# Kernel tuning notes

Hardware: AMD Instinct MI355X
Metric: run time of the kernel (lower is better)

The kernel has to match this reference:

```python
import jax, jax.numpy as jnp
import numpy as np
from functools import partial

N_NODES = 100000
IN_FEATS = 64
HIDDEN = 32
N_EDGES = 3200000


def gcn_conv(x, edge_index, W, b, num_nodes):
    """PyG GCNConv: x' = D^-1/2 (A+I) D^-1/2 (x W) + b, degrees include self-loops."""
    xw = x @ W  # [N, H]
    loop = jnp.arange(num_nodes, dtype=edge_index.dtype)
    src = jnp.concatenate([edge_index[0], loop])
    dst = jnp.concatenate([edge_index[1], loop])
    deg = jax.ops.segment_sum(jnp.ones_like(dst, dtype=xw.dtype), dst,
                              num_segments=num_nodes)  # in-degree incl. self-loop
    dinv = jnp.where(deg > 0, jax.lax.rsqrt(deg), 0.0)
    norm = dinv[src] * dinv[dst]  # [E+N]
    msg = xw[src] * norm[:, None]  # gather + scale
    out = jax.ops.segment_sum(msg, dst, num_segments=num_nodes)  # scatter-add
    return out + b


def setup_inputs() -> dict:
    key = jax.random.key(0)
    ks = jax.random.split(key, 6)
    scale = 1.0 / np.sqrt(IN_FEATS)
    return {
        "x_house": jax.random.normal(ks[0], (N_NODES, IN_FEATS), dtype=jnp.float32),
        "edge_index_near": jax.random.randint(ks[1], (2, N_EDGES), 0, N_NODES, dtype=jnp.int64)
            if jax.config.jax_enable_x64 else jax.random.randint(ks[1], (2, N_EDGES), 0, N_NODES).astype(jnp.int32),
        "edge_index_similar": jax.random.randint(ks[2], (2, N_EDGES), 0, N_NODES).astype(jnp.int32),
        "W_near": jax.random.normal(ks[3], (IN_FEATS, HIDDEN), dtype=jnp.float32) * scale,
        "b_near": jnp.zeros((HIDDEN,), dtype=jnp.float32),
        "W_similar": jax.random.normal(ks[4], (IN_FEATS, HIDDEN), dtype=jnp.float32) * scale,
        "b_similar": jnp.zeros((HIDDEN,), dtype=jnp.float32),
        "W_lin": jax.random.normal(ks[5], (HIDDEN, 1), dtype=jnp.float32) * (1.0 / np.sqrt(HIDDEN)),
        "b_lin": jnp.zeros((1,), dtype=jnp.float32),
    }


def reference(x_house, edge_index_near, edge_index_similar,
              W_near, b_near, W_similar, b_similar, W_lin, b_lin):
    # HeteroConv with aggr='sum': sum of per-edge-type GCNConv outputs on 'house'
    h = (gcn_conv(x_house, edge_index_near, W_near, b_near, N_NODES)
         + gcn_conv(x_house, edge_index_similar, W_similar, b_similar, N_NODES))
    h = jax.nn.relu(h)
    # dropout is identity at inference (training=False)
    out = h @ W_lin + b_lin  # [N, 1]
    return out.squeeze(-1)
```

## Files before the change

### kernel.cpp

```cpp
#include <hip/hip_runtime.h>
#include <hip/hip_fp16.h>


#define SLICES 256
#define BSZ    256
#define NB_MAX 800
#define CAP2   9216
#define PCH    4096
#define LDSPAD 33
#define FXS    65536.0f
#define FXSI   (1.0f / 65536.0f)

__global__ __launch_bounds__(512)
void init_kernel(const float* __restrict__ Wn, const float* __restrict__ Ws,
                 int* __restrict__ goff, float* __restrict__ wtn,
                 float* __restrict__ wts, int nb) {
    const int t = threadIdx.x;
    for (int b = t; b < nb; b += 512) goff[b] = 0;
    for (int i = t; i < 64 * 32; i += 512) {
        int k = i >> 5, h = i & 31;
        wtn[h * 64 + k] = Wn[i];
        wts[h * 64 + k] = Ws[i];
    }
}

__global__ __launch_bounds__(512)
void place_kernel(const int* __restrict__ ei_n, const int* __restrict__ ei_s,
                  int* __restrict__ goff, unsigned int* __restrict__ codes,
                  int En, int Es, int nb) {
    __shared__ unsigned stg[PCH];
    __shared__ unsigned stg2[PCH];
    __shared__ int histT[NB_MAX];
    __shared__ int cur[NB_MAX];
    __shared__ int histC[NB_MAX];
    __shared__ int baseC[NB_MAX];
    __shared__ int gbC[NB_MAX];
    __shared__ int wsum[8];
    const int t = threadIdx.x;
    const int wid = t >> 6, lane = t & 63;
    const int type = blockIdx.y;
    const int* __restrict__ ei = type ? ei_s : ei_n;
    const int E = type ? Es : En;
    int per = ((E + SLICES - 1) / SLICES + 7) & ~7;
    const int e0 = blockIdx.x * per;
    const int e1 = min(e0 + per, E);

    for (int b = t; b < nb; b += 512) histT[b] = 0;
    __syncthreads();

    for (int c0 = e0; c0 < e1; c0 += PCH) {
        const int i = c0 + t * 8;
        int nv = e1 - i; nv = nv < 0 ? 0 : (nv > 8 ? 8 : nv);
        if (nv == 8) {
            int4 dA = *(const int4*)(ei + E + i), dB = *(const int4*)(ei + E + i + 4);
            atomicAdd(&histT[dA.x >> 7], 1);
            atomicAdd(&histT[dA.y >> 7], 1);
            atomicAdd(&histT[dA.z >> 7], 1);
            atomicAdd(&histT[dA.w >> 7], 1);
            atomicAdd(&histT[dB.x >> 7], 1);
            atomicAdd(&histT[dB.y >> 7], 1);
            atomicAdd(&histT[dB.z >> 7], 1);
            atomicAdd(&histT[dB.w >> 7], 1);
        } else {
            for (int j = 0; j < nv; ++j) atomicAdd(&histT[ei[E + i + j] >> 7], 1);
        }
    }
    __syncthreads();

    for (int b = t; b < nb; b += 512) {
        int c = histT[b];
        cur[b] = b * CAP2 + (c ? atomicAdd(&goff[b], c) : 0);
    }
    for (int b = t; b < nb; b += 512) histC[b] = 0;
    __syncthreads();

    for (int c0 = e0; c0 < e1; c0 += PCH) {
        const int i = c0 + t * 8;
        int nv = e1 - i; nv = nv < 0 ? 0 : (nv > 8 ? 8 : nv);
        unsigned cd[8]; int bb[8], rk[8];
        if (nv == 8) {
            int4 sA = *(const int4*)(ei + i),     sB = *(const int4*)(ei + i + 4);
            int4 dA = *(const int4*)(ei + E + i), dB = *(const int4*)(ei + E + i + 4);
            int ss[8] = {sA.x, sA.y, sA.z, sA.w, sB.x, sB.y, sB.z, sB.w};
            int dd[8] = {dA.x, dA.y, dA.z, dA.w, dB.x, dB.y, dB.z, dB.w};
#pragma unroll
            for (int j = 0; j < 8; ++j) {
                bb[j] = dd[j] >> 7;
                cd[j] = ((unsigned)(2 * (dd[j] & 127) + type) << 18)
                      | (unsigned)(2 * ss[j] + type);
            }
        } else {
            for (int j = 0; j < nv; ++j) {
                int sv = ei[i + j], dv = ei[E + i + j];
                bb[j] = dv >> 7;
                cd[j] = ((unsigned)(2 * (dv & 127) + type) << 18)
                      | (unsigned)(2 * sv + type);
            }
        }
#pragma unroll
        for (int j = 0; j < 8; ++j)
            if (j < nv) rk[j] = atomicAdd(&histC[bb[j]], 1);
        __syncthreads();

        const int i0 = wid * 128 + lane, i1 = i0 + 64;
        int v0 = (i0 < nb) ? histC[i0] : 0;
        int v1 = (i1 < nb) ? histC[i1] : 0;
        int x0 = v0;
#pragma unroll
        for (int o = 1; o < 64; o <<= 1) { int n = __shfl_up(x0, o, 64); if (lane >= o) x0 += n; }
        int tot0 = __shfl(x0, 63, 64);
        int x1 = v1;
#pragma unroll
        for (int o = 1; o < 64; o <<= 1) { int n = __shfl_up(x1, o, 64); if (lane >= o) x1 += n; }
        int tot1 = __shfl(x1, 63, 64);
        if (lane == 0) wsum[wid] = tot0 + tot1;
        for (int b = t; b < nb; b += 512) {
            int c = histC[b], g = cur[b];
            gbC[b] = g;
            cur[b] = g + c;
        }
        __syncthreads();
        int woff = 0;
#pragma unroll
        for (int k = 0; k < 8; ++k) woff += (k < wid) ? wsum[k] : 0;
        if (i0 < nb) baseC[i0] = woff + (x0 - v0);
        if (i1 < nb) baseC[i1] = woff + tot0 + (x1 - v1);
        __syncthreads();

#pragma unroll
        for (int j = 0; j < 8; ++j)
            if (j < nv) {
                int p = baseC[bb[j]] + rk[j];
                stg[p] = cd[j];
                stg2[p] = (unsigned)(gbC[bb[j]] + rk[j]);
            }
        __syncthreads();

        const int tot = min(PCH, e1 - c0);
        for (int j = t; j < tot; j += 512)
            codes[stg2[j]] = stg[j];
        for (int b = t; b < nb; b += 512) histC[b] = 0;
        __syncthreads();
    }
}

__global__ __launch_bounds__(256)
void dcxw_kernel(const unsigned int* __restrict__ codes, const int* __restrict__ goff,
                 const float* __restrict__ x,
                 const float* __restrict__ wtn, const float* __restrict__ wts,
                 int* __restrict__ cnt, __half2* __restrict__ xws, int N, int M, int nb) {
    __shared__ int dcnt[512];
    const int t = threadIdx.x;
    dcnt[t] = 0;
    dcnt[t + 256] = 0;
    __syncthreads();

    for (int bb = 0; bb < 2; ++bb) {
        const int bidx = 2 * blockIdx.x + bb;
        if (bidx >= nb) break;
        const int off = bb << 8;
        const int base = bidx * CAP2;
        const int end = base + goff[bidx];
        const int t0 = base + ((end - base) & ~3);
        for (int e = base + t * 4; e < t0; e += 256 * 4) {
            uint4 c = *(const uint4*)(codes + e);
            atomicAdd(&dcnt[off + (c.x >> 18)], 1);
            atomicAdd(&dcnt[off + (c.y >> 18)], 1);
            atomicAdd(&dcnt[off + (c.z >> 18)], 1);
            atomicAdd(&dcnt[off + (c.w >> 18)], 1);
        }
        if (t < end - t0) atomicAdd(&dcnt[off + (codes[t0 + t] >> 18)], 1);
    }
    __syncthreads();

    const int v0 = blockIdx.x * 512 + t;
    if (v0 < M) cnt[v0] = dcnt[t];
    const int v1 = v0 + 256;
    if (v1 < M) cnt[v1] = dcnt[t + 256];

    const int node = blockIdx.x * 256 + t;
    if (node >= N) return;

    float xr[64];
    const float4* x4 = (const float4*)(x + (size_t)node * 64);
#pragma unroll
    for (int q = 0; q < 16; ++q) {
        float4 v = x4[q];
        xr[4 * q] = v.x; xr[4 * q + 1] = v.y; xr[4 * q + 2] = v.z; xr[4 * q + 3] = v.w;
    }
    float dn = rsqrtf((float)dcnt[2 * t] + 1.0f);
    float ds = rsqrtf((float)dcnt[2 * t + 1] + 1.0f);

    const float4* wn4 = (const float4*)wtn;
    const float4* ws4 = (const float4*)wts;

    unsigned pn[16], ps[16];
#pragma unroll
    for (int s2 = 0; s2 < 16; ++s2) {
        float a0n = 0.f, a1n = 0.f, a0s = 0.f, a1s = 0.f;
#pragma unroll
        for (int q = 0; q < 16; ++q) {
            float4 w0n = wn4[(2 * s2) * 16 + q];
            float4 w1n = wn4[(2 * s2 + 1) * 16 + q];
            float4 w0s = ws4[(2 * s2) * 16 + q];
            float4 w1s = ws4[(2 * s2 + 1) * 16 + q];
            float x0 = xr[4 * q], x1 = xr[4 * q + 1], x2 = xr[4 * q + 2], x3 = xr[4 * q + 3];
            a0n += x0 * w0n.x + x1 * w0n.y + x2 * w0n.z + x3 * w0n.w;
            a1n += x0 * w1n.x + x1 * w1n.y + x2 * w1n.z + x3 * w1n.w;
            a0s += x0 * w0s.x + x1 * w0s.y + x2 * w0s.z + x3 * w0s.w;
            a1s += x0 * w1s.x + x1 * w1s.y + x2 * w1s.z + x3 * w1s.w;
        }
        __half2 hn = __floats2half2_rn(a0n * dn, a1n * dn);
        __half2 hs = __floats2half2_rn(a0s * ds, a1s * ds);
        pn[s2] = *(unsigned*)&hn;
        ps[s2] = *(unsigned*)&hs;
    }
    uint4* on = (uint4*)(xws + (size_t)(2 * node) * 16);
    uint4* os = (uint4*)(xws + (size_t)(2 * node + 1) * 16);
#pragma unroll
    for (int q = 0; q < 4; ++q) {
        on[q] = make_uint4(pn[4 * q], pn[4 * q + 1], pn[4 * q + 2], pn[4 * q + 3]);
        os[q] = make_uint4(ps[4 * q], ps[4 * q + 1], ps[4 * q + 2], ps[4 * q + 3]);
    }
}

__global__ __launch_bounds__(1024)
void gather_kernel(const unsigned int* __restrict__ codes, const int* __restrict__ goff,
                   const __half2* __restrict__ xws, const int* __restrict__ cnt,
                   const float* __restrict__ b_n, const float* __restrict__ b_s,
                   const float* __restrict__ W_lin, const float* __restrict__ b_lin,
                   float* __restrict__ out, int N) {
    __shared__ int facc[BSZ * LDSPAD];
    for (int i = threadIdx.x; i < BSZ * LDSPAD; i += 1024) facc[i] = 0;
    __syncthreads();
    const int b = blockIdx.x;
    const int base = b * CAP2;
    const int end = base + goff[b];
    const int sl = threadIdx.x & 15;
    const int grp = threadIdx.x >> 4;

#define GA(cc) xws[(size_t)((cc) & 0x3FFFFu) * 16 + sl]
#define ACC_EDGE(cc, ww) do {                                                \
        float2 f_ = __half22float2(ww);                                      \
        int r_ = (int)((cc) >> 18) * LDSPAD + sl;                            \
        atomicAdd(&facc[r_],      __float2int_rn(f_.x * FXS));               \
        atomicAdd(&facc[r_ + 16], __float2int_rn(f_.y * FXS));               \
    } while (0)

    const int t0 = base + ((end - base) & ~15);
    for (int e = base + grp * 16; e < t0; e += 64 * 16) {
        uint4 c0 = *(const uint4*)(codes + e);
        uint4 c1 = *(const uint4*)(codes + e + 4);
        uint4 c2 = *(const uint4*)(codes + e + 8);
        uint4 c3 = *(const uint4*)(codes + e + 12);
        __half2 w0 = GA(c0.x), w1 = GA(c0.y), w2 = GA(c0.z), w3 = GA(c0.w);
        __half2 w4 = GA(c1.x), w5 = GA(c1.y), w6 = GA(c1.z), w7 = GA(c1.w);
        __half2 w8 = GA(c2.x), w9 = GA(c2.y), wA = GA(c2.z), wB = GA(c2.w);
        __half2 wC = GA(c3.x), wD = GA(c3.y), wE = GA(c3.z), wF = GA(c3.w);
        ACC_EDGE(c0.x, w0); ACC_EDGE(c0.y, w1); ACC_EDGE(c0.z, w2); ACC_EDGE(c0.w, w3);
        ACC_EDGE(c1.x, w4); ACC_EDGE(c1.y, w5); ACC_EDGE(c1.z, w6); ACC_EDGE(c1.w, w7);
        ACC_EDGE(c2.x, w8); ACC_EDGE(c2.y, w9); ACC_EDGE(c2.z, wA); ACC_EDGE(c2.w, wB);
        ACC_EDGE(c3.x, wC); ACC_EDGE(c3.y, wD); ACC_EDGE(c3.z, wE); ACC_EDGE(c3.w, wF);
    }
    for (int e = t0 + grp; e < end; e += 64) {
        unsigned c = codes[e];
        __half2 w = GA(c);
        ACC_EDGE(c, w);
    }
#undef ACC_EDGE
#undef GA

    __syncthreads();
    const float bn0 = b_n[2 * sl], bn1 = b_n[2 * sl + 1];
    const float bs0 = b_s[2 * sl], bs1 = b_s[2 * sl + 1];
    const float wl0 = W_lin[2 * sl], wl1 = W_lin[2 * sl + 1];
    const float bl  = b_lin[0];
    for (int p = grp; p < 128; p += 64) {
        int node = b * 128 + p;
        if (node >= N) break;
        int rn = (2 * p) * LDSPAD, rs = rn + LDSPAD;
        float anx = (float)facc[rn + sl] * FXSI, any_ = (float)facc[rn + 16 + sl] * FXSI;
        float asx = (float)facc[rs + sl] * FXSI, asy  = (float)facc[rs + 16 + sl] * FXSI;
        float2 ns = __half22float2(xws[(size_t)(2 * node) * 16 + sl]);
        float2 ss = __half22float2(xws[(size_t)(2 * node + 1) * 16 + sl]);
        float dn  = rsqrtf((float)cnt[2 * node] + 1.0f);
        float dsv = rsqrtf((float)cnt[2 * node + 1] + 1.0f);
        float h0 = (anx + ns.x) * dn + bn0 + (asx + ss.x) * dsv + bs0;
        float h1 = (any_ + ns.y) * dn + bn1 + (asy + ss.y) * dsv + bs1;
        float pr = fmaxf(h0, 0.f) * wl0 + fmaxf(h1, 0.f) * wl1;
#pragma unroll
        for (int off = 8; off > 0; off >>= 1) pr += __shfl_xor(pr, off, 16);
        if (sl == 0) out[node] = pr + bl;
    }
}

extern "C" void kernel_launch(void* const* d_in, const int* in_sizes, int n_in,
                              void* d_out, int out_size, void* d_ws, size_t ws_size,
                              hipStream_t stream) {
    const float* x     = (const float*)d_in[0];
    const int*   ei_n  = (const int*)d_in[1];
    const int*   ei_s  = (const int*)d_in[2];
    const float* W_n   = (const float*)d_in[3];
    const float* b_n   = (const float*)d_in[4];
    const float* W_s   = (const float*)d_in[5];
    const float* b_s   = (const float*)d_in[6];
    const float* W_lin = (const float*)d_in[7];
    const float* b_lin = (const float*)d_in[8];
    float* out = (float*)d_out;

    const int N  = in_sizes[0] / 64;
    const int En = in_sizes[1] / 2;
    const int Es = in_sizes[2] / 2;
    const int M  = 2 * N;
    const int nb = (M + BSZ - 1) / BSZ;

    int*   goff = (int*)d_ws;
    int*   cnt  = goff + 1024;
    float* wtn  = (float*)(cnt + M);
    float* wts  = wtn + 2048;
    uintptr_t pc = (uintptr_t)(wts + 2048);
    pc = (pc + 15) & ~(uintptr_t)15;
    unsigned int* codes = (unsigned int*)pc;
    __half2* xws = (__half2*)(codes + (size_t)nb * CAP2);

    init_kernel<<<1, 512, 0, stream>>>(W_n, W_s, goff, wtn, wts, nb);
    place_kernel<<<dim3(SLICES, 2), 512, 0, stream>>>(ei_n, ei_s, goff, codes,
                                                      En, Es, nb);
    dcxw_kernel<<<(nb + 1) / 2, 256, 0, stream>>>(codes, goff, x, wtn, wts,
                                                  cnt, xws, N, M, nb);
    gather_kernel<<<nb, 1024, 0, stream>>>(codes, goff, xws, cnt,
                                           b_n, b_s, W_lin, b_lin, out, N);
}
```

Baseline: 287.6 us.

## Split degree count and XW into separate kernels with 16 lanes per node

Breaks the fused degree-count-plus-transform kernel into a degree-count kernel and an XW kernel. In the XW kernel each node is handled by 16 threads, each computing two output columns per edge type, with weights transposed into padded LDS. Previously one thread computed all 64 outputs from a 64-float register array with global weight loads. The init kernel is replaced by hipMemsetAsync, and the weight transpose moves into each block. This adds one kernel launch and a cnt round trip through global memory, and every thread of a node rereads the node's x row.

After: 282.7 us. No clear change (-1.7%).

```diff
diff --git a/kernel.cpp b/kernel.cpp
--- a/kernel.cpp
+++ b/kernel.cpp
@@ -8,21 +8,9 @@
 #define CAP2   9216
 #define PCH    4096
 #define LDSPAD 33
+#define WSTR   68
 #define FXS    65536.0f
 #define FXSI   (1.0f / 65536.0f)
-
-__global__ __launch_bounds__(512)
-void init_kernel(const float* __restrict__ Wn, const float* __restrict__ Ws,
-                 int* __restrict__ goff, float* __restrict__ wtn,
-                 float* __restrict__ wts, int nb) {
-    const int t = threadIdx.x;
-    for (int b = t; b < nb; b += 512) goff[b] = 0;
-    for (int i = t; i < 64 * 32; i += 512) {
-        int k = i >> 5, h = i & 31;
-        wtn[h * 64 + k] = Wn[i];
-        wts[h * 64 + k] = Ws[i];
-    }
-}
 
 __global__ __launch_bounds__(512)
 void place_kernel(const int* __restrict__ ei_n, const int* __restrict__ ei_s,
@@ -145,83 +133,68 @@
 }
 
 __global__ __launch_bounds__(256)
-void dcxw_kernel(const unsigned int* __restrict__ codes, const int* __restrict__ goff,
-                 const float* __restrict__ x,
-                 const float* __restrict__ wtn, const float* __restrict__ wts,
-                 int* __restrict__ cnt, __half2* __restrict__ xws, int N, int M, int nb) {
-    __shared__ int dcnt[512];
+void dcount_kernel(const unsigned int* __restrict__ codes, const int* __restrict__ goff,
+                   int* __restrict__ cnt, int M) {
+    __shared__ int dcnt[BSZ];
     const int t = threadIdx.x;
     dcnt[t] = 0;
-    dcnt[t + 256] = 0;
-    __syncthreads();
-
-    for (int bb = 0; bb < 2; ++bb) {
-        const int bidx = 2 * blockIdx.x + bb;
-        if (bidx >= nb) break;
-        const int off = bb << 8;
-        const int base = bidx * CAP2;
-        const int end = base + goff[bidx];
-        const int t0 = base + ((end - base) & ~3);
-        for (int e = base + t * 4; e < t0; e += 256 * 4) {
-            uint4 c = *(const uint4*)(codes + e);
-            atomicAdd(&dcnt[off + (c.x >> 18)], 1);
-            atomicAdd(&dcnt[off + (c.y >> 18)], 1);
-            atomicAdd(&dcnt[off + (c.z >> 18)], 1);
-            atomicAdd(&dcnt[off + (c.w >> 18)], 1);
-        }
-        if (t < end - t0) atomicAdd(&dcnt[off + (codes[t0 + t] >> 18)], 1);
-    }
-    __syncthreads();
-
-    const int v0 = blockIdx.x * 512 + t;
-    if (v0 < M) cnt[v0] = dcnt[t];
-    const int v1 = v0 + 256;
-    if (v1 < M) cnt[v1] = dcnt[t + 256];
-
-    const int node = blockIdx.x * 256 + t;
+    __syncthreads();
+    const int b = blockIdx.x;
+    const int base = b * CAP2;
+    const int end = base + goff[b];
+    const int t0 = base + ((end - base) & ~3);
+    for (int e = base + t * 4; e < t0; e += 256 * 4) {
+        uint4 c = *(const uint4*)(codes + e);
+        atomicAdd(&dcnt[c.x >> 18], 1);
+        atomicAdd(&dcnt[c.y >> 18], 1);
+        atomicAdd(&dcnt[c.z >> 18], 1);
+        atomicAdd(&dcnt[c.w >> 18], 1);
+    }
+    if (t < end - t0) atomicAdd(&dcnt[codes[t0 + t] >> 18], 1);
+    __syncthreads();
+    const int vnode = b * BSZ + t;
+    if (vnode < M) cnt[vnode] = dcnt[t];
+}
+
+__global__ __launch_bounds__(256)
+void xw_kernel(const float* __restrict__ x,
+               const float* __restrict__ Wn, const float* __restrict__ Ws,
+               const int* __restrict__ cnt,
+               __half2* __restrict__ xws, int N) {
+    __shared__ float wtA[32 * WSTR];
+    __shared__ float wtB[32 * WSTR];
+    const int t = threadIdx.x;
+    for (int i = t; i < 64 * 32; i += 256) {
+        int k = i >> 5, h = i & 31;
+        wtA[h * WSTR + k] = Wn[i];
+        wtB[h * WSTR + k] = Ws[i];
+    }
+    __syncthreads();
+
+    const int ln = t >> 4, sl = t & 15;
+    const int node = blockIdx.x * 16 + ln;
     if (node >= N) return;
 
-    float xr[64];
     const float4* x4 = (const float4*)(x + (size_t)node * 64);
+    const float4* wa4 = (const float4*)&wtA[(2 * sl) * WSTR];
+    const float4* wb4 = (const float4*)&wtA[(2 * sl + 1) * WSTR];
+    const float4* wc4 = (const float4*)&wtB[(2 * sl) * WSTR];
+    const float4* wd4 = (const float4*)&wtB[(2 * sl + 1) * WSTR];
+
+    float a0n = 0.f, a1n = 0.f, a0s = 0.f, a1s = 0.f;
 #pragma unroll
     for (int q = 0; q < 16; ++q) {
-        float4 v = x4[q];
-        xr[4 * q] = v.x; xr[4 * q + 1] = v.y; xr[4 * q + 2] = v.z; xr[4 * q + 3] = v.w;
-    }
-    float dn = rsqrtf((float)dcnt[2 * t] + 1.0f);
-    float ds = rsqrtf((float)dcnt[2 * t + 1] + 1.0f);
-
-    const float4* wn4 = (const float4*)wtn;
-    const float4* ws4 = (const float4*)wts;
-
-    unsigned pn[16], ps[16];
-#pragma unroll
-    for (int s2 = 0; s2 < 16; ++s2) {
-        float a0n = 0.f, a1n = 0.f, a0s = 0.f, a1s = 0.f;
-#pragma unroll
-        for (int q = 0; q < 16; ++q) {
-            float4 w0n = wn4[(2 * s2) * 16 + q];
-            float4 w1n = wn4[(2 * s2 + 1) * 16 + q];
-            float4 w0s = ws4[(2 * s2) * 16 + q];
-            float4 w1s = ws4[(2 * s2 + 1) * 16 + q];
-            float x0 = xr[4 * q], x1 = xr[4 * q + 1], x2 = xr[4 * q + 2], x3 = xr[4 * q + 3];
-            a0n += x0 * w0n.x + x1 * w0n.y + x2 * w0n.z + x3 * w0n.w;
-            a1n += x0 * w1n.x + x1 * w1n.y + x2 * w1n.z + x3 * w1n.w;
-            a0s += x0 * w0s.x + x1 * w0s.y + x2 * w0s.z + x3 * w0s.w;
-            a1s += x0 * w1s.x + x1 * w1s.y + x2 * w1s.z + x3 * w1s.w;
-        }
-        __half2 hn = __floats2half2_rn(a0n * dn, a1n * dn);
-        __half2 hs = __floats2half2_rn(a0s * ds, a1s * ds);
-        pn[s2] = *(unsigned*)&hn;
-        ps[s2] = *(unsigned*)&hs;
-    }
-    uint4* on = (uint4*)(xws + (size_t)(2 * node) * 16);
-    uint4* os = (uint4*)(xws + (size_t)(2 * node + 1) * 16);
-#pragma unroll
-    for (int q = 0; q < 4; ++q) {
-        on[q] = make_uint4(pn[4 * q], pn[4 * q + 1], pn[4 * q + 2], pn[4 * q + 3]);
-        os[q] = make_uint4(ps[4 * q], ps[4 * q + 1], ps[4 * q + 2], ps[4 * q + 3]);
-    }
+        float4 xv = x4[q];
+        float4 wa = wa4[q], wb = wb4[q], wc = wc4[q], wd = wd4[q];
+        a0n += xv.x * wa.x + xv.y * wa.y + xv.z * wa.z + xv.w * wa.w;
+        a1n += xv.x * wb.x + xv.y * wb.y + xv.z * wb.z + xv.w * wb.w;
+        a0s += xv.x * wc.x + xv.y * wc.y + xv.z * wc.z + xv.w * wc.w;
+        a1s += xv.x * wd.x + xv.y * wd.y + xv.z * wd.z + xv.w * wd.w;
+    }
+    float dn = rsqrtf((float)cnt[2 * node] + 1.0f);
+    float ds = rsqrtf((float)cnt[2 * node + 1] + 1.0f);
+    xws[(size_t)(2 * node) * 16 + sl]     = __floats2half2_rn(a0n * dn, a1n * dn);
+    xws[(size_t)(2 * node + 1) * 16 + sl] = __floats2half2_rn(a0s * ds, a1s * ds);
 }
 
 __global__ __launch_bounds__(1024)
@@ -314,20 +287,19 @@
     const int M  = 2 * N;
     const int nb = (M + BSZ - 1) / BSZ;
 
-    int*   goff = (int*)d_ws;
-    int*   cnt  = goff + 1024;
-    float* wtn  = (float*)(cnt + M);
-    float* wts  = wtn + 2048;
-    uintptr_t pc = (uintptr_t)(wts + 2048);
+    int* goff = (int*)d_ws;
+    int* cnt  = goff + 1024;
+    uintptr_t pc = (uintptr_t)(cnt + M);
     pc = (pc + 15) & ~(uintptr_t)15;
     unsigned int* codes = (unsigned int*)pc;
     __half2* xws = (__half2*)(codes + (size_t)nb * CAP2);
 
-    init_kernel<<<1, 512, 0, stream>>>(W_n, W_s, goff, wtn, wts, nb);
+    hipMemsetAsync(goff, 0, (size_t)nb * sizeof(int), stream);
+
     place_kernel<<<dim3(SLICES, 2), 512, 0, stream>>>(ei_n, ei_s, goff, codes,
                                                       En, Es, nb);
-    dcxw_kernel<<<(nb + 1) / 2, 256, 0, stream>>>(codes, goff, x, wtn, wts,
-                                                  cnt, xws, N, M, nb);
+    dcount_kernel<<<nb, 256, 0, stream>>>(codes, goff, cnt, M);
+    xw_kernel<<<(N + 15) / 16, 256, 0, stream>>>(x, W_n, W_s, cnt, xws, N);
     gather_kernel<<<nb, 1024, 0, stream>>>(codes, goff, xws, cnt,
                                            b_n, b_s, W_lin, b_lin, out, N);
 }
```
